# Performance work log

Measured on AMD Instinct MI355X. Metric: run time of the kernel, lower is better.

## Reference

```python
import jax, jax.numpy as jnp
from jax import lax
import numpy as np

B, H, W, C, N = 4, 512, 512, 32, 300000
K, S, P, D = 3, 2, 1, 1  # kernel, stride, padding, dilation


def setup_inputs() -> dict:
    key = jax.random.key(0)
    kf, _ = jax.random.split(key)
    features = jax.random.normal(kf, (N, C), dtype=jnp.float32)
    # unique active coordinates (spconv requires unique sites)
    rng = np.random.default_rng(0)
    lin = rng.choice(B * H * W, size=N, replace=False)
    b = lin // (H * W)
    y = (lin // W) % H
    x = lin % W
    coors = jnp.asarray(np.stack([b, y, x], axis=1), dtype=jnp.int32)  # [N,3]
    return {"features": features, "coors": coors, "batch_size": B}


def reference(features, coors, batch_size):
    # Scatter active features onto a dense grid initialized to -inf so that
    # inputs only; outputs with no active input in window are inactive).
    neg_inf = jnp.array(-jnp.inf, dtype=features.dtype)
    dense = jnp.full((batch_size, H, W, features.shape[1]), neg_inf,
                     dtype=features.dtype)
    b, y, x = coors[:, 0], coors[:, 1], coors[:, 2]
    dense = dense.at[b, y, x].set(features)  # coords are unique
    out = lax.reduce_window(
        dense, neg_inf, lax.max,
        window_dimensions=(1, K, K, 1),
        window_strides=(1, S, S, 1),
        padding=((0, 0), (P, P), (P, P), (0, 0)),
        window_dilation=(1, D, D, 1))
    # inactive output sites -> 0 (dense view of the sparse output tensor)
    return jnp.where(jnp.isinf(out), jnp.zeros((), out.dtype), out)
```

## Files before the change

### kernel.cpp

```cpp
#include <hip/hip_runtime.h>
#include <math.h>

#define BB 4
#define HH 512
#define WW 512
#define CC 32
#define HO 256
#define WO 256

#define MAXOCC 96
#define OVFCAP 100

__global__ void scatter_idx_kernel(const int* __restrict__ coors,
                                   int* __restrict__ grid, int n) {
    int i = blockIdx.x * blockDim.x + threadIdx.x;
    if (i >= n) return;
    int b = coors[i * 3 + 0];
    int y = coors[i * 3 + 1];
    int x = coors[i * 3 + 2];
    grid[((size_t)b * HH + y) * WW + x] = i + 1;
}

__global__ void __launch_bounds__(256, 8)
pool_kernel(const float4* __restrict__ feat,
            const int* __restrict__ grid,
            float4* __restrict__ out,
            int npts) {
    int ox_base = (blockIdx.x & 7) * 32;
    int oy      = (blockIdx.x >> 3) & (HO - 1);
    int b       = blockIdx.x >> 11;

    int tid  = threadIdx.x;
    int lane = tid & 63;
    int cg   = tid & 7;
    int p    = tid >> 3;

    int iy0 = 2 * oy - 1;
    int gx0 = 2 * ox_base - 1;
    const int* gb = grid + (size_t)b * (HH * WW);

    __shared__ int    cnt;
    __shared__ int    smap[3 * 65];
    __shared__ int    srcidx[MAXOCC];
    __shared__ float4 sfeat[MAXOCC * 8];
    __shared__ int    ovf_c[OVFCAP];
    __shared__ int    ovf_i[OVFCAP];

    const float NEG = -INFINITY;
    if (tid == 0) cnt = 0;
    if (tid < 8) sfeat[tid] = make_float4(NEG, NEG, NEG, NEG);
    __syncthreads();

    {
        int v = 0;
        if (tid < 195) {
            int r = tid / 65;
            int c = tid - r * 65;
            int iy = iy0 + r;
            int gx = gx0 + c;
            if ((unsigned)iy < (unsigned)HH && (unsigned)gx < (unsigned)WW) {
                int g = gb[iy * WW + gx];
                if ((unsigned)(g - 1) < (unsigned)npts) v = g;
            }
        }
        unsigned long long mask = __ballot(v != 0);
        int nz = (int)__popcll(mask);
        int base = 0;
        if (lane == 0 && nz) base = atomicAdd(&cnt, nz);
        base = __shfl(base, 0);
        int s = 1 + base + (int)__popcll(mask & ((1ull << lane) - 1ull));
        if (tid < 195) {
            int m = 0;
            if (v != 0) {
                if (s < MAXOCC) { srcidx[s] = v - 1; m = s; }
                else {
                    int o = s - MAXOCC;
                    ovf_c[o] = tid;
                    ovf_i[o] = v - 1;
                }
            }
            smap[tid] = m;
        }
    }
    __syncthreads();

    int hi = cnt < (MAXOCC - 1) ? cnt : (MAXOCC - 1);
    for (int s = 1 + (tid >> 3); s <= hi; s += 32)
        sfeat[(s << 3) + ((cg + s) & 7)] = feat[(size_t)srcidx[s] * 8 + cg];
    __syncthreads();

    int lc = 2 * p;
    float4 acc = make_float4(NEG, NEG, NEG, NEG);
#pragma unroll
    for (int r = 0; r < 3; ++r) {
        int m0 = smap[r * 65 + lc + 0];
        int m1 = smap[r * 65 + lc + 1];
        int m2 = smap[r * 65 + lc + 2];
        float4 f0 = sfeat[(m0 << 3) + ((cg + m0) & 7)];
        float4 f1 = sfeat[(m1 << 3) + ((cg + m1) & 7)];
        float4 f2 = sfeat[(m2 << 3) + ((cg + m2) & 7)];
        acc.x = fmaxf(fmaxf(acc.x, f0.x), fmaxf(f1.x, f2.x));
        acc.y = fmaxf(fmaxf(acc.y, f0.y), fmaxf(f1.y, f2.y));
        acc.z = fmaxf(fmaxf(acc.z, f0.z), fmaxf(f1.z, f2.z));
        acc.w = fmaxf(fmaxf(acc.w, f0.w), fmaxf(f1.w, f2.w));
    }

    if (cnt >= MAXOCC) {
        int novf = cnt - (MAXOCC - 1);
        if (novf > OVFCAP) novf = OVFCAP;
        for (int o = 0; o < novf; ++o) {
            int cell = ovf_c[o];
            int c = cell % 65;
            if (c >= lc && c <= lc + 2) {
                float4 fv = feat[(size_t)ovf_i[o] * 8 + cg];
                acc.x = fmaxf(acc.x, fv.x);
                acc.y = fmaxf(acc.y, fv.y);
                acc.z = fmaxf(acc.z, fv.z);
                acc.w = fmaxf(acc.w, fv.w);
            }
        }
    }

    acc.x = isinf(acc.x) ? 0.0f : acc.x;
    acc.y = isinf(acc.y) ? 0.0f : acc.y;
    acc.z = isinf(acc.z) ? 0.0f : acc.z;
    acc.w = isinf(acc.w) ? 0.0f : acc.w;

    size_t pos = ((size_t)(b * HO + oy) * WO + ox_base + p);
    out[pos * 8 + cg] = acc;
}

extern "C" void kernel_launch(void* const* d_in, const int* in_sizes, int n_in,
                              void* d_out, int out_size, void* d_ws, size_t ws_size,
                              hipStream_t stream) {
    const float* features = (const float*)d_in[0];
    const int*   coors    = (const int*)d_in[1];
    int n = in_sizes[0] / CC;

    int* grid = (int*)d_ws;

    {
        int blk = 256, grd = (n + blk - 1) / blk;
        scatter_idx_kernel<<<grd, blk, 0, stream>>>(coors, grid, n);
    }
    {
        int grd = BB * HO * (WO / 32);
        pool_kernel<<<grd, 256, 0, stream>>>((const float4*)features, grid,
                                             (float4*)d_out, n);
    }
}
```

Before: 103.2 us.

## Process four output rows per block to reuse overlapping input rows

Each pool block now covers four output rows instead of one. It loads a 9x65 window of grid cells and their features into shared memory once and computes four output rows from it. Adjacent output rows share one input row, so this cuts redundant grid lookups and feature gathers from about three input rows per output row to about 2.25. Shared-memory capacity is raised (MAXOCC 256, larger overflow buffer) and occupancy hint lowered to 4, so there are fewer blocks, each using more LDS, and the overflow scan is repeated per output row.

```diff
diff --git a/kernel.cpp b/kernel.cpp
--- a/kernel.cpp
+++ b/kernel.cpp
@@ -8,8 +8,13 @@
 #define HO 256
 #define WO 256
 
-#define MAXOCC 96
-#define OVFCAP 100
+#define ROWS 9
+#define COLS 65
+#define CELLS (ROWS * COLS)
+#define OYPB 4
+
+#define MAXOCC 256
+#define OVFCAP 330
 
 __global__ void scatter_idx_kernel(const int* __restrict__ coors,
                                    int* __restrict__ grid, int n) {
@@ -21,26 +26,26 @@
     grid[((size_t)b * HH + y) * WW + x] = i + 1;
 }
 
-__global__ void __launch_bounds__(256, 8)
+__global__ void __launch_bounds__(256, 4)
 pool_kernel(const float4* __restrict__ feat,
             const int* __restrict__ grid,
             float4* __restrict__ out,
             int npts) {
     int ox_base = (blockIdx.x & 7) * 32;
-    int oy      = (blockIdx.x >> 3) & (HO - 1);
-    int b       = blockIdx.x >> 11;
+    int oy_base = ((blockIdx.x >> 3) & 63) * OYPB;
+    int b       = blockIdx.x >> 9;
 
     int tid  = threadIdx.x;
     int lane = tid & 63;
     int cg   = tid & 7;
     int p    = tid >> 3;
 
-    int iy0 = 2 * oy - 1;
+    int iy0 = 2 * oy_base - 1;
     int gx0 = 2 * ox_base - 1;
     const int* gb = grid + (size_t)b * (HH * WW);
 
     __shared__ int    cnt;
-    __shared__ int    smap[3 * 65];
+    __shared__ int    smap[CELLS];
     __shared__ int    srcidx[MAXOCC];
     __shared__ float4 sfeat[MAXOCC * 8];
     __shared__ int    ovf_c[OVFCAP];
@@ -51,17 +56,15 @@
     if (tid < 8) sfeat[tid] = make_float4(NEG, NEG, NEG, NEG);
     __syncthreads();
 
-    {
+    for (int cell = tid; cell < CELLS; cell += 256) {
         int v = 0;
-        if (tid < 195) {
-            int r = tid / 65;
-            int c = tid - r * 65;
-            int iy = iy0 + r;
-            int gx = gx0 + c;
-            if ((unsigned)iy < (unsigned)HH && (unsigned)gx < (unsigned)WW) {
-                int g = gb[iy * WW + gx];
-                if ((unsigned)(g - 1) < (unsigned)npts) v = g;
-            }
+        int r = cell / COLS;
+        int c = cell - r * COLS;
+        int iy = iy0 + r;
+        int gx = gx0 + c;
+        if ((unsigned)iy < (unsigned)HH && (unsigned)gx < (unsigned)WW) {
+            int g = gb[iy * WW + gx];
+            if ((unsigned)(g - 1) < (unsigned)npts) v = g;
         }
         unsigned long long mask = __ballot(v != 0);
         int nz = (int)__popcll(mask);
@@ -69,18 +72,16 @@
         if (lane == 0 && nz) base = atomicAdd(&cnt, nz);
         base = __shfl(base, 0);
         int s = 1 + base + (int)__popcll(mask & ((1ull << lane) - 1ull));
-        if (tid < 195) {
-            int m = 0;
-            if (v != 0) {
-                if (s < MAXOCC) { srcidx[s] = v - 1; m = s; }
-                else {
-                    int o = s - MAXOCC;
-                    ovf_c[o] = tid;
-                    ovf_i[o] = v - 1;
-                }
+        int m = 0;
+        if (v != 0) {
+            if (s < MAXOCC) { srcidx[s] = v - 1; m = s; }
+            else {
+                int o = s - MAXOCC;
+                ovf_c[o] = cell;
+                ovf_i[o] = v - 1;
             }
-            smap[tid] = m;
         }
+        smap[cell] = m;
     }
     __syncthreads();
 
@@ -90,44 +91,55 @@
     __syncthreads();
 
     int lc = 2 * p;
-    float4 acc = make_float4(NEG, NEG, NEG, NEG);
-#pragma unroll
-    for (int r = 0; r < 3; ++r) {
-        int m0 = smap[r * 65 + lc + 0];
-        int m1 = smap[r * 65 + lc + 1];
-        int m2 = smap[r * 65 + lc + 2];
-        float4 f0 = sfeat[(m0 << 3) + ((cg + m0) & 7)];
-        float4 f1 = sfeat[(m1 << 3) + ((cg + m1) & 7)];
-        float4 f2 = sfeat[(m2 << 3) + ((cg + m2) & 7)];
-        acc.x = fmaxf(fmaxf(acc.x, f0.x), fmaxf(f1.x, f2.x));
-        acc.y = fmaxf(fmaxf(acc.y, f0.y), fmaxf(f1.y, f2.y));
-        acc.z = fmaxf(fmaxf(acc.z, f0.z), fmaxf(f1.z, f2.z));
-        acc.w = fmaxf(fmaxf(acc.w, f0.w), fmaxf(f1.w, f2.w));
+    bool ovf = (cnt >= MAXOCC);
+    int novf = 0;
+    if (ovf) {
+        novf = cnt - (MAXOCC - 1);
+        if (novf > OVFCAP) novf = OVFCAP;
     }
 
-    if (cnt >= MAXOCC) {
-        int novf = cnt - (MAXOCC - 1);
-        if (novf > OVFCAP) novf = OVFCAP;
-        for (int o = 0; o < novf; ++o) {
-            int cell = ovf_c[o];
-            int c = cell % 65;
-            if (c >= lc && c <= lc + 2) {
-                float4 fv = feat[(size_t)ovf_i[o] * 8 + cg];
-                acc.x = fmaxf(acc.x, fv.x);
-                acc.y = fmaxf(acc.y, fv.y);
-                acc.z = fmaxf(acc.z, fv.z);
-                acc.w = fmaxf(acc.w, fv.w);
+#pragma unroll
+    for (int oyl = 0; oyl < OYPB; ++oyl) {
+        float4 acc = make_float4(NEG, NEG, NEG, NEG);
+#pragma unroll
+        for (int dr = 0; dr < 3; ++dr) {
+            int r = 2 * oyl + dr;
+            int m0 = smap[r * COLS + lc + 0];
+            int m1 = smap[r * COLS + lc + 1];
+            int m2 = smap[r * COLS + lc + 2];
+            float4 f0 = sfeat[(m0 << 3) + ((cg + m0) & 7)];
+            float4 f1 = sfeat[(m1 << 3) + ((cg + m1) & 7)];
+            float4 f2 = sfeat[(m2 << 3) + ((cg + m2) & 7)];
+            acc.x = fmaxf(fmaxf(acc.x, f0.x), fmaxf(f1.x, f2.x));
+            acc.y = fmaxf(fmaxf(acc.y, f0.y), fmaxf(f1.y, f2.y));
+            acc.z = fmaxf(fmaxf(acc.z, f0.z), fmaxf(f1.z, f2.z));
+            acc.w = fmaxf(fmaxf(acc.w, f0.w), fmaxf(f1.w, f2.w));
+        }
+
+        if (ovf) {
+            for (int o = 0; o < novf; ++o) {
+                int cell = ovf_c[o];
+                int r = cell / COLS;
+                int c = cell - r * COLS;
+                if (c >= lc && c <= lc + 2 &&
+                    r >= 2 * oyl && r <= 2 * oyl + 2) {
+                    float4 fv = feat[(size_t)ovf_i[o] * 8 + cg];
+                    acc.x = fmaxf(acc.x, fv.x);
+                    acc.y = fmaxf(acc.y, fv.y);
+                    acc.z = fmaxf(acc.z, fv.z);
+                    acc.w = fmaxf(acc.w, fv.w);
+                }
             }
         }
+
+        acc.x = isinf(acc.x) ? 0.0f : acc.x;
+        acc.y = isinf(acc.y) ? 0.0f : acc.y;
+        acc.z = isinf(acc.z) ? 0.0f : acc.z;
+        acc.w = isinf(acc.w) ? 0.0f : acc.w;
+
+        size_t pos = ((size_t)(b * HO + oy_base + oyl) * WO + ox_base + p);
+        out[pos * 8 + cg] = acc;
     }
-
-    acc.x = isinf(acc.x) ? 0.0f : acc.x;
-    acc.y = isinf(acc.y) ? 0.0f : acc.y;
-    acc.z = isinf(acc.z) ? 0.0f : acc.z;
-    acc.w = isinf(acc.w) ? 0.0f : acc.w;
-
-    size_t pos = ((size_t)(b * HO + oy) * WO + ox_base + p);
-    out[pos * 8 + cg] = acc;
 }
 
 extern "C" void kernel_launch(void* const* d_in, const int* in_sizes, int n_in,
@@ -144,7 +156,7 @@
         scatter_idx_kernel<<<grd, blk, 0, stream>>>(coors, grid, n);
     }
     {
-        int grd = BB * HO * (WO / 32);
+        int grd = BB * (HO / OYPB) * (WO / 32);
         pool_kernel<<<grd, 256, 0, stream>>>((const float4*)features, grid,
                                              (float4*)d_out, n);
     }
```

After: 105.0 us. About the same (+1.7%).
